# Kernel tuning notes

Measured on AMD Instinct MI355X. Metric: run time of the kernel, lower is better.

## Reference

```python
import jax, jax.numpy as jnp
import numpy as np

N_NODES = 100000
N_EDGES = 3200000
HID = 52
N_LAYERS = 3


def setup_inputs() -> dict:
    key = jax.random.key(0)
    ks = jax.random.split(key, 6)
    x = jax.random.normal(ks[0], (N_NODES, HID), dtype=jnp.float32)
    edge_index = jax.random.randint(ks[1], (2, N_EDGES), 0, N_NODES, dtype=jnp.int32)
    w1 = jax.random.normal(ks[2], (N_LAYERS, HID, 2 * HID), dtype=jnp.float32) * 0.1
    b1 = jnp.zeros((N_LAYERS, 2 * HID), dtype=jnp.float32)
    w2 = jax.random.normal(ks[3], (N_LAYERS, 2 * HID, HID), dtype=jnp.float32) * 0.1
    b2 = jnp.zeros((N_LAYERS, HID), dtype=jnp.float32)
    eps = jnp.zeros((N_LAYERS,), dtype=jnp.float32)
    lin_w = jax.random.normal(ks[4], (HID * (N_LAYERS + 1), HID), dtype=jnp.float32) * 0.1
    lin_b = jnp.zeros((HID,), dtype=jnp.float32)
    return {"x": x, "edge_index": edge_index, "w1": w1, "b1": b1,
            "w2": w2, "b2": b2, "eps": eps, "lin_w": lin_w, "lin_b": lin_b}


def reference(x, edge_index, w1, b1, w2, b2, eps, lin_w, lin_b):
    src, dst = edge_index[0], edge_index[1]
    n = x.shape[0]
    h = x
    h_list = [x]
    for l in range(N_LAYERS):
        # GINConv: sum-aggregate neighbor features at target nodes
        agg = jax.ops.segment_sum(h[src], dst, num_segments=n)  # [N, HID]
        z = (1.0 + eps[l]) * h + agg
        # 2-layer MLP: Linear -> ReLU -> Linear
        z = jnp.maximum(z @ w1[l] + b1[l], 0.0) @ w2[l] + b2[l]
        # outer ReLU (dropout p=0 is identity)
        h = jnp.maximum(z, 0.0)
        h_list.append(h)
    node_repr = jnp.concatenate(h_list, axis=1)  # [N, HID*(L+1)]
    return node_repr @ lin_w + lin_b
```

## Files before the change

### kernel.cpp

```cpp
#include <hip/hip_runtime.h>

#define HID 52
#define HID2 104
#define P1_CHUNK 8192
#define NBIN_MAX 512
#define HSTRIDE 136

typedef unsigned short ushort_t;
typedef unsigned int uint_t;
typedef short bf16x8 __attribute__((ext_vector_type(8)));
typedef float f32x4 __attribute__((ext_vector_type(4)));
typedef float f32x2 __attribute__((ext_vector_type(2)));

__device__ __forceinline__ ushort_t f2bf(float f) {
    union { float f; uint_t u; } c; c.f = f;
    uint_t u = c.u + 0x7FFFu + ((c.u >> 16) & 1u);
    return (ushort_t)(u >> 16);
}
__device__ __forceinline__ float bflo(uint_t u) {
    union { uint_t u; float f; } c; c.u = u << 16; return c.f;
}
__device__ __forceinline__ float bfhi(uint_t u) {
    union { uint_t u; float f; } c; c.u = u & 0xFFFF0000u; return c.f;
}
__device__ __forceinline__ f32x2 unpk(uint_t u) {
    return (f32x2){bflo(u), bfhi(u)};
}

__global__ __launch_bounds__(256) void setup_kernel(const float* __restrict__ x,
                                                    const float* __restrict__ w1,
                                                    const float* __restrict__ w2,
                                                    const float* __restrict__ lin_w,
                                                    const int* __restrict__ dst,
                                                    ushort_t* __restrict__ xb,
                                                    ushort_t* __restrict__ h1b,
                                                    ushort_t* __restrict__ h2b,
                                                    ushort_t* __restrict__ h3b,
                                                    ushort_t* __restrict__ w1f,
                                                    ushort_t* __restrict__ w2f,
                                                    ushort_t* __restrict__ linf,
                                                    int* __restrict__ ghist,
                                                    int n, int E, int nxblk) {
    __shared__ int lh[NBIN_MAX];
    int blk = blockIdx.x;
    int tid = threadIdx.x;
    if (blk < nxblk) {
        int t = blk * 256 + tid;
        if (t >= n * 16) return;
        int node = t >> 4, pp = t & 15;
        int c0 = pp * 4;
        ushort_t o[4];
#pragma unroll
        for (int j = 0; j < 4; j++) {
            int c = c0 + j;
            o[j] = (c < HID) ? f2bf(x[(size_t)node * HID + c]) : 0;
        }
        uint_t u0 = (uint_t)o[0] | ((uint_t)o[1] << 16);
        uint_t u1 = (uint_t)o[2] | ((uint_t)o[3] << 16);
        *(uint2*)(xb + (size_t)node * 64 + c0) = make_uint2(u0, u1);
        return;
    }
    if (blk == nxblk) {
        ushort_t* arr = (tid < 64) ? xb : (tid < 128) ? h1b : (tid < 192) ? h2b : h3b;
        arr[(size_t)n * 64 + (tid & 63)] = 0;
        return;
    }
    if (blk < nxblk + 32) {
        int gid = (blk - nxblk - 1) * 4 + (tid >> 6);
        int lane = tid & 63;
        if (gid >= 122) return;
        int m = lane & 15, q = lane >> 4;
        ushort_t o[8];
        ushort_t* dstp;
        if (gid < 42) {
            int l = gid / 14, r = gid % 14, ct = r >> 1, ks = r & 1;
            int nn = ct * 16 + m;
#pragma unroll
            for (int j = 0; j < 8; j++) {
                int k = ks * 32 + q * 8 + j;
                o[j] = (k < HID && nn < HID2) ? f2bf(w1[((size_t)l * HID + k) * HID2 + nn]) : 0;
            }
            dstp = w1f + ((size_t)(l * 14 + ct * 2 + ks) * 64 + lane) * 8;
        } else if (gid < 90) {
            int g2 = gid - 42, l = g2 / 16, r = g2 % 16, ct = r >> 2, ks = r & 3;
            int nn = ct * 16 + m;
#pragma unroll
            for (int j = 0; j < 8; j++) {
                int k = ks * 32 + q * 8 + j;
                o[j] = (k < HID2 && nn < HID) ? f2bf(w2[((size_t)l * HID2 + k) * HID + nn]) : 0;
            }
            dstp = w2f + ((size_t)(l * 16 + ct * 4 + ks) * 64 + lane) * 8;
        } else {
            int g2 = gid - 90, ct = g2 >> 3, ks = g2 & 7;
            int nn = ct * 16 + m;
#pragma unroll
            for (int j = 0; j < 8; j++) {
                int kg = ks * 32 + q * 8 + j;
                int seg = kg >> 6, kk = kg & 63;
                o[j] = (kk < HID && nn < HID) ? f2bf(lin_w[((size_t)seg * HID + kk) * HID + nn]) : 0;
            }
            dstp = linf + ((size_t)(ct * 8 + ks) * 64 + lane) * 8;
        }
        uint4 u;
        u.x = (uint_t)o[0] | ((uint_t)o[1] << 16);
        u.y = (uint_t)o[2] | ((uint_t)o[3] << 16);
        u.z = (uint_t)o[4] | ((uint_t)o[5] << 16);
        u.w = (uint_t)o[6] | ((uint_t)o[7] << 16);
        *(uint4*)dstp = u;
        return;
    }
    int eblk = blk - nxblk - 32;
    lh[tid] = 0; lh[tid + 256] = 0;
    __syncthreads();
    int base = eblk * P1_CHUNK;
    int cend = min(P1_CHUNK, E - base);
    for (int i = tid; i < cend; i += 256) atomicAdd(&lh[dst[base + i] >> 8], 1);
    __syncthreads();
    int cc = lh[tid];       if (cc) atomicAdd(&ghist[tid], cc);
    cc = lh[tid + 256];     if (cc) atomicAdd(&ghist[tid + 256], cc);
}

__global__ __launch_bounds__(256) void pass1_kernel(const int* __restrict__ src,
                                                    const int* __restrict__ dst,
                                                    const int* __restrict__ ghist,
                                                    int* __restrict__ gcnt,
                                                    uint_t* __restrict__ packed, int E) {
    __shared__ uint_t stage[P1_CHUNK];
    __shared__ ushort_t sbin[P1_CHUNK];
    __shared__ int gh[NBIN_MAX];
    __shared__ int cnt[NBIN_MAX];
    __shared__ int sst[NBIN_MAX];
    __shared__ int curs[NBIN_MAX];
    __shared__ int gbase[NBIN_MAX];
    __shared__ int ps[256];
    int tid = threadIdx.x;
    int b0 = 2 * tid, b1 = 2 * tid + 1;
    gh[b0] = ghist[b0]; gh[b1] = ghist[b1];
    cnt[tid] = 0; cnt[tid + 256] = 0;
    __syncthreads();
    int gpair = gh[b0] + gh[b1];
    ps[tid] = gpair;
    __syncthreads();
    for (int off = 1; off < 256; off <<= 1) {
        int t = (tid >= off) ? ps[tid - off] : 0;
        __syncthreads();
        ps[tid] += t;
        __syncthreads();
    }
    int bst0 = ps[tid] - gpair;
    int bst1 = bst0 + gh[b0];
    __syncthreads();
    int base = blockIdx.x * P1_CHUNK;
    int cend = min(P1_CHUNK, E - base);
    for (int i = tid; i < cend; i += 256) atomicAdd(&cnt[dst[base + i] >> 8], 1);
    __syncthreads();
    int c0 = cnt[b0], c1 = cnt[b1];
    int pair = c0 + c1;
    ps[tid] = pair;
    __syncthreads();
    for (int off = 1; off < 256; off <<= 1) {
        int t = (tid >= off) ? ps[tid - off] : 0;
        __syncthreads();
        ps[tid] += t;
        __syncthreads();
    }
    int ex = ps[tid] - pair;
    sst[b0] = ex;       curs[b0] = ex;
    sst[b1] = ex + c0;  curs[b1] = ex + c0;
    gbase[b0] = c0 ? (bst0 + atomicAdd(&gcnt[b0], c0)) : 0;
    gbase[b1] = c1 ? (bst1 + atomicAdd(&gcnt[b1], c1)) : 0;
    __syncthreads();
    for (int i = tid; i < cend; i += 256) {
        int d = dst[base + i];
        int s = src[base + i];
        int b = d >> 8;
        int pos = atomicAdd(&curs[b], 1);
        stage[pos] = ((uint_t)s << 8) | (uint_t)(d & 255);
        sbin[pos] = (ushort_t)b;
    }
    __syncthreads();
    for (int i = tid; i < cend; i += 256) {
        int b = sbin[i];
        packed[gbase[b] + (i - sst[b])] = stage[i];
    }
}

__global__ __launch_bounds__(256) void pass2_kernel(const uint_t* __restrict__ packed,
                                                    const int* __restrict__ ghist,
                                                    int* __restrict__ srcsorted,
                                                    int* __restrict__ nrs,
                                                    int* __restrict__ ndeg, int N) {
    __shared__ int c[NBIN_MAX];
    __shared__ int ps[256];
    __shared__ int hist[1024];
    __shared__ int curs[1024];
    int b = blockIdx.x;
    int tid = threadIdx.x;
    int b0 = 2 * tid, b1 = 2 * tid + 1;
    c[b0] = ghist[b0]; c[b1] = ghist[b1];
    hist[tid] = 0; hist[tid + 256] = 0; hist[tid + 512] = 0; hist[tid + 768] = 0;
    __syncthreads();
    int gpair = c[b0] + c[b1];
    ps[tid] = gpair;
    __syncthreads();
    for (int off = 1; off < 256; off <<= 1) {
        int t = (tid >= off) ? ps[tid - off] : 0;
        __syncthreads();
        ps[tid] += t;
        __syncthreads();
    }
    int e0 = ps[tid] - gpair;
    int cntb0 = c[b0], cntb1 = c[b1];
    __syncthreads();
    c[b0] = e0;
    c[b1] = e0 + cntb0;
    __syncthreads();
    int beg = c[b];
    int cntb = (b == b0) ? cntb0 : 0;
    cntb = ghist[b];
    int end = beg + cntb;
    int obase = beg + b * 4096;
    for (int i = beg + tid; i < end; i += 256) {
        uint_t p = packed[i];
        int key = ((int)(p & 255u) << 2) | (int)((p >> 8) >> 15);
        atomicAdd(&hist[key], 1);
    }
    __syncthreads();
    int h0 = hist[tid * 4], h1 = hist[tid * 4 + 1], h2 = hist[tid * 4 + 2], h3 = hist[tid * 4 + 3];
    int v = h0 + h1 + h2 + h3;
    int pv = (v + 15) & ~15;
    ps[tid] = pv;
    __syncthreads();
    for (int off = 1; off < 256; off <<= 1) {
        int t = (tid >= off) ? ps[tid - off] : 0;
        __syncthreads();
        ps[tid] += t;
        __syncthreads();
    }
    int start = obase + ps[tid] - pv;
    int node = b * 256 + tid;
    if (node < N) { nrs[node] = start; ndeg[node] = pv; }
    curs[tid * 4 + 0] = start;
    curs[tid * 4 + 1] = start + h0;
    curs[tid * 4 + 2] = start + h0 + h1;
    curs[tid * 4 + 3] = start + h0 + h1 + h2;
    __syncthreads();
    for (int i = beg + tid; i < end; i += 256) {
        uint_t p = packed[i];
        int s = (int)(p >> 8);
        int key = ((int)(p & 255u) << 2) | (s >> 15);
        int pos = atomicAdd(&curs[key], 1);
        srcsorted[pos] = s;
    }
    __syncthreads();
    for (int i = start + v; i < start + pv; i++) srcsorted[i] = N;
}

__global__ __launch_bounds__(256) void agg_kernel(const ushort_t* __restrict__ hb,
                                                  const int* __restrict__ nrs,
                                                  const int* __restrict__ ndeg,
                                                  const int* __restrict__ srcsorted,
                                                  const float* __restrict__ eps,
                                                  ushort_t* __restrict__ zb, int n) {
    int wid = (blockIdx.x * blockDim.x + threadIdx.x) >> 6;
    if (wid >= n) return;
    int lane = threadIdx.x & 63;
    int g = lane >> 3, sub = lane & 7;
    int beg = nrs[wid];
    int total = ndeg[wid];
    const ushort_t* hsub = hb + sub * 8;
    const int* ss = srcsorted + beg + g;

    f32x2 A0 = {0,0}, A1 = {0,0}, A2 = {0,0}, A3 = {0,0};
    f32x2 B0 = {0,0}, B1 = {0,0}, B2 = {0,0}, B3 = {0,0};
    if (total > 0) {
        int f0 = ss[0], f1 = ss[8], f2r = ss[16], f3r = ss[24];
        for (int b = 0; b < total; b += 32) {
            bool ok = (b + 16) < total;
            int e0 = f0, e1 = f1;
            int e2 = ok ? f2r : n;
            int e3 = ok ? f3r : n;
            f0 = ss[b + 32]; f1 = ss[b + 40]; f2r = ss[b + 48]; f3r = ss[b + 56];
            uint4 v0 = *(const uint4*)(hsub + (size_t)e0 * 64);
            uint4 v1 = *(const uint4*)(hsub + (size_t)e1 * 64);
            uint4 v2 = *(const uint4*)(hsub + (size_t)e2 * 64);
            uint4 v3 = *(const uint4*)(hsub + (size_t)e3 * 64);
            A0 += unpk(v0.x); A1 += unpk(v0.y); A2 += unpk(v0.z); A3 += unpk(v0.w);
            B0 += unpk(v1.x); B1 += unpk(v1.y); B2 += unpk(v1.z); B3 += unpk(v1.w);
            A0 += unpk(v2.x); A1 += unpk(v2.y); A2 += unpk(v2.z); A3 += unpk(v2.w);
            B0 += unpk(v3.x); B1 += unpk(v3.y); B2 += unpk(v3.z); B3 += unpk(v3.w);
        }
    }
    A0 += B0; A1 += B1; A2 += B2; A3 += B3;
    float a0 = A0.x, a1 = A0.y, a2 = A1.x, a3 = A1.y;
    float a4 = A2.x, a5 = A2.y, a6 = A3.x, a7 = A3.y;
#pragma unroll
    for (int msk = 8; msk <= 32; msk <<= 1) {
        a0 += __shfl_xor(a0, msk); a1 += __shfl_xor(a1, msk);
        a2 += __shfl_xor(a2, msk); a3 += __shfl_xor(a3, msk);
        a4 += __shfl_xor(a4, msk); a5 += __shfl_xor(a5, msk);
        a6 += __shfl_xor(a6, msk); a7 += __shfl_xor(a7, msk);
    }
    if (lane < 8) {
        float sc = 1.0f + eps[0];
        uint4 sv = *(const uint4*)(hb + (size_t)wid * 64 + lane * 8);
        float o0 = fmaf(sc, bflo(sv.x), a0), o1 = fmaf(sc, bfhi(sv.x), a1);
        float o2 = fmaf(sc, bflo(sv.y), a2), o3 = fmaf(sc, bfhi(sv.y), a3);
        float o4 = fmaf(sc, bflo(sv.z), a4), o5 = fmaf(sc, bfhi(sv.z), a5);
        float o6 = fmaf(sc, bflo(sv.w), a6), o7 = fmaf(sc, bfhi(sv.w), a7);
        uint4 u;
        u.x = (uint_t)f2bf(o0) | ((uint_t)f2bf(o1) << 16);
        u.y = (uint_t)f2bf(o2) | ((uint_t)f2bf(o3) << 16);
        u.z = (uint_t)f2bf(o4) | ((uint_t)f2bf(o5) << 16);
        u.w = (uint_t)f2bf(o6) | ((uint_t)f2bf(o7) << 16);
        *(uint4*)(zb + (size_t)wid * 64 + lane * 8) = u;
    }
}

__global__ __launch_bounds__(256) void mlp_kernel(const ushort_t* __restrict__ zb,
                                                  const ushort_t* __restrict__ w1f,
                                                  const float* __restrict__ b1,
                                                  const ushort_t* __restrict__ w2f,
                                                  const float* __restrict__ b2,
                                                  ushort_t* __restrict__ hbout, int n) {
    __shared__ ushort_t hid[64 * HSTRIDE];
    int tid = threadIdx.x;
    int w = tid >> 6, lane = tid & 63, m = lane & 15, q = lane >> 4;
    for (int i = tid; i < 64 * 32; i += 256) {
        int r = i >> 5, c = HID2 + (i & 31);
        hid[r * HSTRIDE + c] = 0;
    }
    __syncthreads();

    int nb = blockIdx.x * 64 + w * 16;
    f32x4 acc1[7];
#pragma unroll
    for (int ct = 0; ct < 7; ct++) {
        int col = ct * 16 + m;
        float bv = (col < HID2) ? b1[col] : 0.f;
        acc1[ct] = (f32x4){bv, bv, bv, bv};
    }
    int anode = min(nb + m, n - 1);
#pragma unroll
    for (int ks = 0; ks < 2; ks++) {
        bf16x8 a = *(const bf16x8*)(zb + (size_t)anode * 64 + ks * 32 + q * 8);
#pragma unroll
        for (int ct = 0; ct < 7; ct++) {
            bf16x8 b = *(const bf16x8*)(w1f + ((size_t)(ct * 2 + ks) * 64 + lane) * 8);
            acc1[ct] = __builtin_amdgcn_mfma_f32_16x16x32_bf16(a, b, acc1[ct], 0, 0, 0);
        }
    }
#pragma unroll
    for (int ct = 0; ct < 7; ct++) {
#pragma unroll
        for (int r = 0; r < 4; r++) {
            float v = fmaxf(acc1[ct][r], 0.f);
            int row = w * 16 + q * 4 + r;
            hid[row * HSTRIDE + ct * 16 + m] = f2bf(v);
        }
    }
    f32x4 acc2[4];
#pragma unroll
    for (int ct = 0; ct < 4; ct++) {
        int col = ct * 16 + m;
        float bv = (col < HID) ? b2[col] : 0.f;
        acc2[ct] = (f32x4){bv, bv, bv, bv};
    }
#pragma unroll
    for (int ks = 0; ks < 4; ks++) {
        bf16x8 a = *(const bf16x8*)&hid[(w * 16 + m) * HSTRIDE + ks * 32 + q * 8];
#pragma unroll
        for (int ct = 0; ct < 4; ct++) {
            bf16x8 b = *(const bf16x8*)(w2f + ((size_t)(ct * 4 + ks) * 64 + lane) * 8);
            acc2[ct] = __builtin_amdgcn_mfma_f32_16x16x32_bf16(a, b, acc2[ct], 0, 0, 0);
        }
    }
#pragma unroll
    for (int ct = 0; ct < 4; ct++) {
#pragma unroll
        for (int r = 0; r < 4; r++) {
            int node = nb + q * 4 + r;
            if (node < n) {
                float v = fmaxf(acc2[ct][r], 0.f);
                hbout[(size_t)node * 64 + ct * 16 + m] = f2bf(v);
            }
        }
    }
}

__global__ __launch_bounds__(256) void final_kernel(const ushort_t* __restrict__ xb,
                                                    const ushort_t* __restrict__ h1b,
                                                    const ushort_t* __restrict__ h2b,
                                                    const ushort_t* __restrict__ h3b,
                                                    const ushort_t* __restrict__ linf,
                                                    const float* __restrict__ lin_b,
                                                    float* __restrict__ out, int ntiles) {
    int tid = threadIdx.x;
    int w = tid >> 6, lane = tid & 63, m = lane & 15, q = lane >> 4;
    int tile = blockIdx.x * 4 + w;
    if (tile >= ntiles) return;
    int nb = tile * 16;
    const ushort_t* segs[4] = {xb, h1b, h2b, h3b};
    f32x4 acc[4];
#pragma unroll
    for (int ct = 0; ct < 4; ct++) {
        int col = ct * 16 + m;
        float bv = (col < HID) ? lin_b[col] : 0.f;
        acc[ct] = (f32x4){bv, bv, bv, bv};
    }
#pragma unroll
    for (int ks = 0; ks < 8; ks++) {
        const ushort_t* p = segs[ks >> 1];
        bf16x8 a = *(const bf16x8*)(p + (size_t)(nb + m) * 64 + (ks & 1) * 32 + q * 8);
#pragma unroll
        for (int ct = 0; ct < 4; ct++) {
            bf16x8 b = *(const bf16x8*)(linf + ((size_t)(ct * 8 + ks) * 64 + lane) * 8);
            acc[ct] = __builtin_amdgcn_mfma_f32_16x16x32_bf16(a, b, acc[ct], 0, 0, 0);
        }
    }
#pragma unroll
    for (int ct = 0; ct < 4; ct++) {
        int col = ct * 16 + m;
        if (col < HID) {
#pragma unroll
            for (int r = 0; r < 4; r++)
                out[(size_t)(nb + q * 4 + r) * HID + col] = acc[ct][r];
        }
    }
}

extern "C" void kernel_launch(void* const* d_in, const int* in_sizes, int n_in,
                              void* d_out, int out_size, void* d_ws, size_t ws_size,
                              hipStream_t stream) {
    const float* x     = (const float*)d_in[0];
    const int*   ei    = (const int*)d_in[1];
    const float* w1    = (const float*)d_in[2];
    const float* b1    = (const float*)d_in[3];
    const float* w2    = (const float*)d_in[4];
    const float* b2    = (const float*)d_in[5];
    const float* eps   = (const float*)d_in[6];
    const float* lin_w = (const float*)d_in[7];
    const float* lin_b = (const float*)d_in[8];
    float* out = (float*)d_out;

    const int N = in_sizes[0] / HID;
    const int E = in_sizes[1] / 2;
    const int* src = ei;
    const int* dst = ei + E;

    const int NBIN = (N + 255) / 256;

    char* p = (char*)d_ws;
    const size_t ROWS = (size_t)(N + 1) * 64 * 2;
    ushort_t* xb  = (ushort_t*)p;  p += ROWS;
    ushort_t* zb  = (ushort_t*)p;  p += ROWS;
    ushort_t* h1b = (ushort_t*)p;  p += ROWS;
    ushort_t* h2b = (ushort_t*)p;  p += ROWS;
    ushort_t* h3b = (ushort_t*)p;  p += ROWS;
    ushort_t* w1f = (ushort_t*)p;  p += 3 * 14 * 512 * 2;
    ushort_t* w2f = (ushort_t*)p;  p += 3 * 16 * 512 * 2;
    ushort_t* linf= (ushort_t*)p;  p += 32 * 512 * 2;
    int* ghist    = (int*)p;       p += 512 * 4;
    int* gcnt     = (int*)p;       p += 512 * 4;
    int* nrs      = (int*)p;       p += (size_t)(N + 4) * 4;
    int* ndeg     = (int*)p;       p += (size_t)(N + 4) * 4;
    uint_t* packed = (uint_t*)p;   p += (size_t)E * 4;
    int* srcsorted = (int*)p;

    ushort_t* hbs[4] = {xb, h1b, h2b, h3b};

    const int BLK = 256;
    const int NP1 = (E + P1_CHUNK - 1) / P1_CHUNK;
    const int NXBLK = (N * 16 + BLK - 1) / BLK;
    const int NBUCK = (N + 63) / 64;
    dim3 blk(BLK);
    dim3 grid_agg(((size_t)N * 64 + BLK - 1) / BLK);

    hipMemsetAsync(ghist, 0, 1024 * sizeof(int), stream);
    setup_kernel<<<NXBLK + 32 + NP1, blk, 0, stream>>>(x, w1, w2, lin_w, dst,
                                                       xb, h1b, h2b, h3b,
                                                       w1f, w2f, linf, ghist, N, E, NXBLK);
    pass1_kernel<<<NP1, blk, 0, stream>>>(src, dst, ghist, gcnt, packed, E);
    pass2_kernel<<<NBIN, blk, 0, stream>>>(packed, ghist, srcsorted, nrs, ndeg, N);

    for (int l = 0; l < 3; l++) {
        agg_kernel<<<grid_agg, blk, 0, stream>>>(hbs[l], nrs, ndeg, srcsorted, eps + l, zb, N);
        mlp_kernel<<<NBUCK, blk, 0, stream>>>(zb,
                                              w1f + (size_t)l * 14 * 512,
                                              b1 + (size_t)l * HID2,
                                              w2f + (size_t)l * 16 * 512,
                                              b2 + (size_t)l * HID,
                                              hbs[l + 1], N);
    }
    final_kernel<<<(6250 + 3) / 4 + 1, blk, 0, stream>>>(xb, h1b, h2b, h3b, linf, lin_b,
                                                         out, (N + 15) / 16);
}
```

Baseline: 407.3 us.

## Fuse final linear projection into last-layer MLP kernel and simplify pass2 bucketing

The final concat-linear projection now runs inside the last MLP kernel: layer-3 activations stay in shared memory instead of being written to an h3 buffer and read back by a separate final kernel. That removes one launch and a full round trip of h3 through global memory. The pass2 sort now keys on the low destination byte only, with a 256-entry histogram instead of a 1024-entry sub-keyed one, which drops the secondary source-range ordering inside each node's edge list. A bf16 unpack helper is also simplified, and the LAST kernel variant uses more shared memory.

```diff
diff --git a/kernel.cpp b/kernel.cpp
--- a/kernel.cpp
+++ b/kernel.cpp
@@ -23,8 +23,10 @@
 __device__ __forceinline__ float bfhi(uint_t u) {
     union { uint_t u; float f; } c; c.u = u & 0xFFFF0000u; return c.f;
 }
-__device__ __forceinline__ f32x2 unpk(uint_t u) {
-    return (f32x2){bflo(u), bfhi(u)};
+__device__ __forceinline__ f32x2 unpk2(uint_t u) {
+    union { uint_t u; float f; } lo, hi;
+    lo.u = u << 16; hi.u = u;
+    return (f32x2){lo.f, hi.f};
 }
 
 __global__ __launch_bounds__(256) void setup_kernel(const float* __restrict__ x,
@@ -35,7 +37,6 @@
                                                     ushort_t* __restrict__ xb,
                                                     ushort_t* __restrict__ h1b,
                                                     ushort_t* __restrict__ h2b,
-                                                    ushort_t* __restrict__ h3b,
                                                     ushort_t* __restrict__ w1f,
                                                     ushort_t* __restrict__ w2f,
                                                     ushort_t* __restrict__ linf,
@@ -61,7 +62,7 @@
         return;
     }
     if (blk == nxblk) {
-        ushort_t* arr = (tid < 64) ? xb : (tid < 128) ? h1b : (tid < 192) ? h2b : h3b;
+        ushort_t* arr = (tid < 64) ? xb : (tid < 128) ? h1b : h2b;
         arr[(size_t)n * 64 + (tid & 63)] = 0;
         return;
     }
@@ -192,15 +193,14 @@
                                                     int* __restrict__ ndeg, int N) {
     __shared__ int c[NBIN_MAX];
     __shared__ int ps[256];
-    __shared__ int hist[1024];
-    __shared__ int curs[1024];
+    __shared__ int hist[256];
+    __shared__ int curs[256];
     int b = blockIdx.x;
     int tid = threadIdx.x;
     int b0 = 2 * tid, b1 = 2 * tid + 1;
-    c[b0] = ghist[b0]; c[b1] = ghist[b1];
-    hist[tid] = 0; hist[tid + 256] = 0; hist[tid + 512] = 0; hist[tid + 768] = 0;
-    __syncthreads();
-    int gpair = c[b0] + c[b1];
+    int g0 = ghist[b0], g1 = ghist[b1];
+    hist[tid] = 0;
+    int gpair = g0 + g1;
     ps[tid] = gpair;
     __syncthreads();
     for (int off = 1; off < 256; off <<= 1) {
@@ -209,25 +209,16 @@
         ps[tid] += t;
         __syncthreads();
     }
-    int e0 = ps[tid] - gpair;
-    int cntb0 = c[b0], cntb1 = c[b1];
-    __syncthreads();
-    c[b0] = e0;
-    c[b1] = e0 + cntb0;
+    int ex = ps[tid] - gpair;
+    c[b0] = ex;
+    c[b1] = ex + g0;
     __syncthreads();
     int beg = c[b];
-    int cntb = (b == b0) ? cntb0 : 0;
-    cntb = ghist[b];
-    int end = beg + cntb;
+    int end = beg + ghist[b];
     int obase = beg + b * 4096;
-    for (int i = beg + tid; i < end; i += 256) {
-        uint_t p = packed[i];
-        int key = ((int)(p & 255u) << 2) | (int)((p >> 8) >> 15);
-        atomicAdd(&hist[key], 1);
-    }
-    __syncthreads();
-    int h0 = hist[tid * 4], h1 = hist[tid * 4 + 1], h2 = hist[tid * 4 + 2], h3 = hist[tid * 4 + 3];
-    int v = h0 + h1 + h2 + h3;
+    for (int i = beg + tid; i < end; i += 256) atomicAdd(&hist[packed[i] & 255u], 1);
+    __syncthreads();
+    int v = hist[tid];
     int pv = (v + 15) & ~15;
     ps[tid] = pv;
     __syncthreads();
@@ -240,17 +231,12 @@
     int start = obase + ps[tid] - pv;
     int node = b * 256 + tid;
     if (node < N) { nrs[node] = start; ndeg[node] = pv; }
-    curs[tid * 4 + 0] = start;
-    curs[tid * 4 + 1] = start + h0;
-    curs[tid * 4 + 2] = start + h0 + h1;
-    curs[tid * 4 + 3] = start + h0 + h1 + h2;
+    curs[tid] = start;
     __syncthreads();
     for (int i = beg + tid; i < end; i += 256) {
         uint_t p = packed[i];
-        int s = (int)(p >> 8);
-        int key = ((int)(p & 255u) << 2) | (s >> 15);
-        int pos = atomicAdd(&curs[key], 1);
-        srcsorted[pos] = s;
+        int pos = atomicAdd(&curs[p & 255u], 1);
+        srcsorted[pos] = (int)(p >> 8);
     }
     __syncthreads();
     for (int i = start + v; i < start + pv; i++) srcsorted[i] = N;
@@ -285,10 +271,10 @@
             uint4 v1 = *(const uint4*)(hsub + (size_t)e1 * 64);
             uint4 v2 = *(const uint4*)(hsub + (size_t)e2 * 64);
             uint4 v3 = *(const uint4*)(hsub + (size_t)e3 * 64);
-            A0 += unpk(v0.x); A1 += unpk(v0.y); A2 += unpk(v0.z); A3 += unpk(v0.w);
-            B0 += unpk(v1.x); B1 += unpk(v1.y); B2 += unpk(v1.z); B3 += unpk(v1.w);
-            A0 += unpk(v2.x); A1 += unpk(v2.y); A2 += unpk(v2.z); A3 += unpk(v2.w);
-            B0 += unpk(v3.x); B1 += unpk(v3.y); B2 += unpk(v3.z); B3 += unpk(v3.w);
+            A0 += unpk2(v0.x); A1 += unpk2(v0.y); A2 += unpk2(v0.z); A3 += unpk2(v0.w);
+            B0 += unpk2(v1.x); B1 += unpk2(v1.y); B2 += unpk2(v1.z); B3 += unpk2(v1.w);
+            A0 += unpk2(v2.x); A1 += unpk2(v2.y); A2 += unpk2(v2.z); A3 += unpk2(v2.w);
+            B0 += unpk2(v3.x); B1 += unpk2(v3.y); B2 += unpk2(v3.z); B3 += unpk2(v3.w);
         }
     }
     A0 += B0; A1 += B1; A2 += B2; A3 += B3;
@@ -317,13 +303,21 @@
     }
 }
 
+template<int LAST>
 __global__ __launch_bounds__(256) void mlp_kernel(const ushort_t* __restrict__ zb,
                                                   const ushort_t* __restrict__ w1f,
                                                   const float* __restrict__ b1,
                                                   const ushort_t* __restrict__ w2f,
                                                   const float* __restrict__ b2,
-                                                  ushort_t* __restrict__ hbout, int n) {
+                                                  ushort_t* __restrict__ hbout,
+                                                  const ushort_t* __restrict__ xb,
+                                                  const ushort_t* __restrict__ h1b,
+                                                  const ushort_t* __restrict__ h2b,
+                                                  const ushort_t* __restrict__ linf,
+                                                  const float* __restrict__ lin_b,
+                                                  float* __restrict__ out, int n) {
     __shared__ ushort_t hid[64 * HSTRIDE];
+    __shared__ ushort_t h3t[LAST ? 64 * 68 : 1];
     int tid = threadIdx.x;
     int w = tid >> 6, lane = tid & 63, m = lane & 15, q = lane >> 4;
     for (int i = tid; i < 64 * 32; i += 256) {
@@ -375,56 +369,62 @@
             acc2[ct] = __builtin_amdgcn_mfma_f32_16x16x32_bf16(a, b, acc2[ct], 0, 0, 0);
         }
     }
-#pragma unroll
-    for (int ct = 0; ct < 4; ct++) {
-#pragma unroll
-        for (int r = 0; r < 4; r++) {
-            int node = nb + q * 4 + r;
-            if (node < n) {
+
+    if (!LAST) {
+#pragma unroll
+        for (int ct = 0; ct < 4; ct++) {
+#pragma unroll
+            for (int r = 0; r < 4; r++) {
+                int node = nb + q * 4 + r;
+                if (node < n) {
+                    float v = fmaxf(acc2[ct][r], 0.f);
+                    hbout[(size_t)node * 64 + ct * 16 + m] = f2bf(v);
+                }
+            }
+        }
+    } else {
+#pragma unroll
+        for (int ct = 0; ct < 4; ct++) {
+#pragma unroll
+            for (int r = 0; r < 4; r++) {
                 float v = fmaxf(acc2[ct][r], 0.f);
-                hbout[(size_t)node * 64 + ct * 16 + m] = f2bf(v);
-            }
-        }
-    }
-}
-
-__global__ __launch_bounds__(256) void final_kernel(const ushort_t* __restrict__ xb,
-                                                    const ushort_t* __restrict__ h1b,
-                                                    const ushort_t* __restrict__ h2b,
-                                                    const ushort_t* __restrict__ h3b,
-                                                    const ushort_t* __restrict__ linf,
-                                                    const float* __restrict__ lin_b,
-                                                    float* __restrict__ out, int ntiles) {
-    int tid = threadIdx.x;
-    int w = tid >> 6, lane = tid & 63, m = lane & 15, q = lane >> 4;
-    int tile = blockIdx.x * 4 + w;
-    if (tile >= ntiles) return;
-    int nb = tile * 16;
-    const ushort_t* segs[4] = {xb, h1b, h2b, h3b};
-    f32x4 acc[4];
-#pragma unroll
-    for (int ct = 0; ct < 4; ct++) {
-        int col = ct * 16 + m;
-        float bv = (col < HID) ? lin_b[col] : 0.f;
-        acc[ct] = (f32x4){bv, bv, bv, bv};
-    }
-#pragma unroll
-    for (int ks = 0; ks < 8; ks++) {
-        const ushort_t* p = segs[ks >> 1];
-        bf16x8 a = *(const bf16x8*)(p + (size_t)(nb + m) * 64 + (ks & 1) * 32 + q * 8);
+                h3t[(w * 16 + q * 4 + r) * 68 + ct * 16 + m] = f2bf(v);
+            }
+        }
+        f32x4 accF[4];
 #pragma unroll
         for (int ct = 0; ct < 4; ct++) {
-            bf16x8 b = *(const bf16x8*)(linf + ((size_t)(ct * 8 + ks) * 64 + lane) * 8);
-            acc[ct] = __builtin_amdgcn_mfma_f32_16x16x32_bf16(a, b, acc[ct], 0, 0, 0);
-        }
-    }
-#pragma unroll
-    for (int ct = 0; ct < 4; ct++) {
-        int col = ct * 16 + m;
-        if (col < HID) {
-#pragma unroll
-            for (int r = 0; r < 4; r++)
-                out[(size_t)(nb + q * 4 + r) * HID + col] = acc[ct][r];
+            int col = ct * 16 + m;
+            float bv = (col < HID) ? lin_b[col] : 0.f;
+            accF[ct] = (f32x4){bv, bv, bv, bv};
+        }
+        const ushort_t* segs[3] = {xb, h1b, h2b};
+#pragma unroll
+        for (int ks = 0; ks < 8; ks++) {
+            bf16x8 a;
+            if (ks < 6) {
+                const ushort_t* p = segs[ks >> 1];
+                a = *(const bf16x8*)(p + (size_t)anode * 64 + (ks & 1) * 32 + q * 8);
+            } else {
+                a = *(const bf16x8*)&h3t[(w * 16 + m) * 68 + (ks & 1) * 32 + q * 8];
+            }
+#pragma unroll
+            for (int ct = 0; ct < 4; ct++) {
+                bf16x8 b = *(const bf16x8*)(linf + ((size_t)(ct * 8 + ks) * 64 + lane) * 8);
+                accF[ct] = __builtin_amdgcn_mfma_f32_16x16x32_bf16(a, b, accF[ct], 0, 0, 0);
+            }
+        }
+#pragma unroll
+        for (int ct = 0; ct < 4; ct++) {
+            int col = ct * 16 + m;
+            if (col < HID) {
+#pragma unroll
+                for (int r = 0; r < 4; r++) {
+                    int node = nb + q * 4 + r;
+                    if (node < n)
+                        out[(size_t)node * HID + col] = accF[ct][r];
+                }
+            }
         }
     }
 }
@@ -456,7 +456,6 @@
     ushort_t* zb  = (ushort_t*)p;  p += ROWS;
     ushort_t* h1b = (ushort_t*)p;  p += ROWS;
     ushort_t* h2b = (ushort_t*)p;  p += ROWS;
-    ushort_t* h3b = (ushort_t*)p;  p += ROWS;
     ushort_t* w1f = (ushort_t*)p;  p += 3 * 14 * 512 * 2;
     ushort_t* w2f = (ushort_t*)p;  p += 3 * 16 * 512 * 2;
     ushort_t* linf= (ushort_t*)p;  p += 32 * 512 * 2;
@@ -467,7 +466,7 @@
     uint_t* packed = (uint_t*)p;   p += (size_t)E * 4;
     int* srcsorted = (int*)p;
 
-    ushort_t* hbs[4] = {xb, h1b, h2b, h3b};
+    ushort_t* hbs[3] = {xb, h1b, h2b};
 
     const int BLK = 256;
     const int NP1 = (E + P1_CHUNK - 1) / P1_CHUNK;
@@ -478,20 +477,29 @@
 
     hipMemsetAsync(ghist, 0, 1024 * sizeof(int), stream);
     setup_kernel<<<NXBLK + 32 + NP1, blk, 0, stream>>>(x, w1, w2, lin_w, dst,
-                                                       xb, h1b, h2b, h3b,
+                                                       xb, h1b, h2b,
                                                        w1f, w2f, linf, ghist, N, E, NXBLK);
     pass1_kernel<<<NP1, blk, 0, stream>>>(src, dst, ghist, gcnt, packed, E);
     pass2_kernel<<<NBIN, blk, 0, stream>>>(packed, ghist, srcsorted, nrs, ndeg, N);
 
-    for (int l = 0; l < 3; l++) {
+    for (int l = 0; l < 2; l++) {
         agg_kernel<<<grid_agg, blk, 0, stream>>>(hbs[l], nrs, ndeg, srcsorted, eps + l, zb, N);
-        mlp_kernel<<<NBUCK, blk, 0, stream>>>(zb,
-                                              w1f + (size_t)l * 14 * 512,
-                                              b1 + (size_t)l * HID2,
-                                              w2f + (size_t)l * 16 * 512,
-                                              b2 + (size_t)l * HID,
-                                              hbs[l + 1], N);
-    }
-    final_kernel<<<(6250 + 3) / 4 + 1, blk, 0, stream>>>(xb, h1b, h2b, h3b, linf, lin_b,
-                                                         out, (N + 15) / 16);
-}
+        mlp_kernel<0><<<NBUCK, blk, 0, stream>>>(zb,
+                                                 w1f + (size_t)l * 14 * 512,
+                                                 b1 + (size_t)l * HID2,
+                                                 w2f + (size_t)l * 16 * 512,
+                                                 b2 + (size_t)l * HID,
+                                                 hbs[l + 1],
+                                                 nullptr, nullptr, nullptr,
+                                                 nullptr, nullptr, nullptr, N);
+    }
+    agg_kernel<<<grid_agg, blk, 0, stream>>>(h2b, nrs, ndeg, srcsorted, eps + 2, zb, N);
+    mlp_kernel<1><<<NBUCK, blk, 0, stream>>>(zb,
+                                             w1f + 2 * 14 * 512,
+                                             b1 + 2 * HID2,
+                                             w2f + 2 * 16 * 512,
+                                             b2 + 2 * HID,
+                                             nullptr,
+                                             xb, h1b, h2b,
+                                             linf, lin_b, out, N);
+}
```

Result: faster. 397.4 us (-2.4%).
